# Kernel tuning notes

Hardware: AMD Instinct MI355X
Metric: run time of the kernel (lower is better)

The kernel has to match this reference:

```python
import jax, jax.numpy as jnp
import numpy as np

B, S, H, NH, DH, F, L = 4, 2048, 512, 8, 64, 2048, 4
ALPHA = 1.0   # config.lag_time_scale_alpha
EPS = 1e-12   # BERT layer_norm_eps
MS_PER_MIN = 60.0 * 1000.0


def setup_inputs() -> dict:
    key = jax.random.key(0)
    ks = jax.random.split(key, 24)
    p = lambda k, shape: (jax.random.normal(k, shape, jnp.float32) * 0.02)
    inp = {
        "query_states": jax.random.normal(ks[0], (B, S, H), jnp.float32),
        "attention_mask": jnp.zeros((B, 1, 1, S), jnp.float32),
        "position_bias": jax.random.normal(ks[1], (1, NH, S, S), jnp.float32) * 0.02,
        "timestamp": jnp.sort(jax.random.randint(ks[2], (B, S), 0, 36_000_000, jnp.int32), axis=-1),
        # stacked per-layer parameters (L leading dim)
        "wq": p(ks[3], (L, H, H)), "bq": jnp.zeros((L, H), jnp.float32),
        "wk": p(ks[4], (L, H, H)), "bk": jnp.zeros((L, H), jnp.float32),
        "wv": p(ks[5], (L, H, H)), "bv": jnp.zeros((L, H), jnp.float32),
        "wo": p(ks[6], (L, H, H)), "bo": jnp.zeros((L, H), jnp.float32),
        "ln1_g": jnp.ones((L, H), jnp.float32), "ln1_b": jnp.zeros((L, H), jnp.float32),
        "wi": p(ks[7], (L, H, F)), "bi": jnp.zeros((L, F), jnp.float32),
        "wo2": p(ks[8], (L, F, H)), "bo2": jnp.zeros((L, H), jnp.float32),
        "ln2_g": jnp.ones((L, H), jnp.float32), "ln2_b": jnp.zeros((L, H), jnp.float32),
    }
    return inp


def _ln(x, g, b):
    m = x.mean(-1, keepdims=True)
    v = ((x - m) ** 2).mean(-1, keepdims=True)
    return (x - m) / jnp.sqrt(v + EPS) * g + b


def reference(query_states, attention_mask, position_bias, timestamp,
              wq, bq, wk, bk, wv, bv, wo, bo, ln1_g, ln1_b,
              wi, bi, wo2, bo2, ln2_g, ln2_b):
    # encoder (is_decoder=False) lag-time scale: (B,1,S,S)
    lag = (timestamp[:, None, :, None] - timestamp[:, None, None, :]).astype(jnp.float32) / MS_PER_MIN
    scale = np.sqrt(DH).astype(np.float32) - ALPHA / (jnp.clip(lag, 0.0) + 1.0) + ALPHA

    x = query_states
    for l in range(L):
        def proj(w, b):
            return (x @ w + b).reshape(B, S, NH, DH).transpose(0, 2, 1, 3)  # (B,NH,S,DH)
        q, k, v = proj(wq[l], bq[l]), proj(wk[l], bk[l]), proj(wv[l], bv[l])
        scores = jnp.einsum('bhqd,bhkd->bhqk', q, k) / scale + position_bias + attention_mask
        probs = jax.nn.softmax(scores, axis=-1)
        ctx = jnp.einsum('bhqk,bhkd->bhqd', probs, v).transpose(0, 2, 1, 3).reshape(B, S, H)
        attn = _ln(ctx @ wo[l] + bo[l] + x, ln1_g[l], ln1_b[l])
        ffn = jax.nn.gelu(attn @ wi[l] + bi[l], approximate=False) @ wo2[l] + bo2[l]
        x = _ln(ffn + attn, ln2_g[l], ln2_b[l])
    return x
```

## Files before the change

kernel.cpp:

```cpp
#include <hip/hip_runtime.h>
#include <stdint.h>

typedef unsigned short u16;
using short8  = __attribute__((ext_vector_type(8))) short;
using float4v = __attribute__((ext_vector_type(4))) float;

#define L2E 1.4426950408889634f

__device__ inline float4v f4zero() { float4v z = {0.f, 0.f, 0.f, 0.f}; return z; }

__device__ inline u16 f2bf(float f) {
  union { float f; uint32_t i; } v; v.f = f;
  uint32_t r = v.i + 0x7fffu + ((v.i >> 16) & 1u);
  return (u16)(r >> 16);
}
__device__ inline float bf2f(u16 h) {
  union { uint32_t i; float f; } v; v.i = ((uint32_t)h) << 16; return v.f;
}

__device__ inline void glds16(const u16* g, u16* lds_base, int lane) {
#if __has_builtin(__builtin_amdgcn_global_load_lds)
  (void)lane;
  __builtin_amdgcn_global_load_lds((const __attribute__((address_space(1))) void*)g,
                                   (__attribute__((address_space(3))) void*)lds_base,
                                   16, 0, 0);
#else
  *(uint4*)(lds_base + (size_t)lane * 8) = *(const uint4*)g;
#endif
}

__global__ __launch_bounds__(256) void transpose_cast_kernel(
    const float* __restrict__ in, u16* __restrict__ out, int K, int N, size_t out_ls) {
  __shared__ float tile[32][33];
  const int tx = threadIdx.x & 31, ty = threadIdx.x >> 5;
  in  += (size_t)blockIdx.z * K * N;
  out += (size_t)blockIdx.z * out_ls;
  const int n  = blockIdx.x * 32 + tx;
  const int k0 = blockIdx.y * 32;
#pragma unroll
  for (int j = 0; j < 32; j += 8)
    tile[ty + j][tx] = in[(size_t)(k0 + ty + j) * N + n];
  __syncthreads();
  const int k = k0 + tx;
  const int n0 = blockIdx.x * 32;
#pragma unroll
  for (int j = 0; j < 32; j += 8)
    out[(size_t)(n0 + ty + j) * K + k] = f2bf(tile[tx][ty + j]);
}

__global__ __launch_bounds__(256) void cast_kernel(const float* __restrict__ in,
                                                   u16* __restrict__ out) {
  const int i = (blockIdx.x * 256 + threadIdx.x) * 4;
  float4 t = *(const float4*)(in + i);
  ushort4 o;
  o.x = f2bf(t.x); o.y = f2bf(t.y); o.z = f2bf(t.z); o.w = f2bf(t.w);
  *(ushort4*)(out + i) = o;
}

__global__ __launch_bounds__(256) void pb_tile_kernel(const float* __restrict__ pb,
                                                      u16* __restrict__ pbT) {
  const int g  = blockIdx.x * 256 + threadIdx.x;
  const int mm = g & 15;
  const int q  = (g >> 4) & 2047;
  const int kbh = g >> 15;
  const int kb = kbh & 31, h = kbh >> 5;
  const float* src = pb + ((size_t)h * 2048 + q) * 2048 + kb * 64 + mm;
  ushort4 o;
  o.x = f2bf(src[0]  * L2E);
  o.y = f2bf(src[16] * L2E);
  o.z = f2bf(src[32] * L2E);
  o.w = f2bf(src[48] * L2E);
  *(ushort4*)(pbT + ((size_t)(h * 32 + kb) * 2048 + q) * 64 + mm * 4) = o;
}

__global__ __launch_bounds__(256) void maskts_kernel(const float* __restrict__ mask,
                                                     const int* __restrict__ ts,
                                                     float* __restrict__ maskE,
                                                     float* __restrict__ tsf) {
  const int i = blockIdx.x * 256 + threadIdx.x;
  maskE[i] = mask[i] * L2E;
  tsf[i]   = (float)ts[i];
}

template <int BM, int BN, int NN, int KK, int EPI>
__global__ __launch_bounds__(256) void gemm_kernel(
    const u16* __restrict__ A, const u16* __restrict__ Wt,
    const float* __restrict__ b0, const float* __restrict__ b1, const float* __restrict__ b2,
    const u16* __restrict__ resid,
    void* __restrict__ o0, void* __restrict__ o1, void* __restrict__ o2) {
  constexpr int FI = BM / 32;
  constexpr int FJB = BN / 32;
  constexpr int FIW = BM / 32;
  constexpr int FJW = BN / 32;
  __shared__ __align__(16) u16 As[BM * 64];
  __shared__ __align__(16) u16 Bs[BN * 64];
  const int tid = threadIdx.x, lane = tid & 63, wv = tid >> 6;
  const int quad = lane >> 4, mm = lane & 15;
  const int m0 = blockIdx.x * BM, n0 = blockIdx.y * BN;
  const int wm = (wv >> 1) * (BM / 2), wn = (wv & 1) * (BN / 2);
  const int srow = tid >> 3, slot = tid & 7;
  const int chunk = slot ^ (srow & 7);
  const u16* Ag = A  + (size_t)(m0 + srow) * KK + chunk * 8;
  const u16* Bg = Wt + (size_t)(n0 + srow) * KK + chunk * 8;
  u16* AsW = As + (size_t)(wv * 8) * 64;
  u16* BsW = Bs + (size_t)(wv * 8) * 64;
  const int sw = mm & 7;

  float4v acc[FIW][FJW];
#pragma unroll
  for (int i = 0; i < FIW; i++)
#pragma unroll
    for (int j = 0; j < FJW; j++) acc[i][j] = f4zero();

  for (int kt = 0; kt < KK; kt += 64) {
#pragma unroll
    for (int i = 0; i < FI; i++)
      glds16(Ag + (size_t)i * 32 * KK + kt, AsW + i * 32 * 64, lane);
#pragma unroll
    for (int j = 0; j < FJB; j++)
      glds16(Bg + (size_t)j * 32 * KK + kt, BsW + j * 32 * 64, lane);
    __syncthreads();
#pragma unroll
    for (int ks = 0; ks < 2; ks++) {
      short8 a[FIW], b[FJW];
#pragma unroll
      for (int i = 0; i < FIW; i++)
        a[i] = *(const short8*)(As + (size_t)(wm + i * 16 + mm) * 64 + (size_t)((ks * 4 + quad) ^ sw) * 8);
#pragma unroll
      for (int j = 0; j < FJW; j++)
        b[j] = *(const short8*)(Bs + (size_t)(wn + j * 16 + mm) * 64 + (size_t)((ks * 4 + quad) ^ sw) * 8);
#pragma unroll
      for (int i = 0; i < FIW; i++)
#pragma unroll
        for (int j = 0; j < FJW; j++)
          acc[i][j] = __builtin_amdgcn_mfma_f32_16x16x32_bf16(a[i], b[j], acc[i][j], 0, 0, 0);
    }
    __syncthreads();
  }

#pragma unroll
  for (int j = 0; j < FJW; j++) {
    const int gn = n0 + wn + j * 16 + mm;
    if (EPI == 4) {
      const int which = gn >> 9, col = gn & 511, h = (gn >> 6) & 7, d = gn & 63;
      const float* bp = (which == 0) ? b0 : (which == 1) ? b1 : b2;
      const float bias = bp[col];
      u16* dst = (which == 0) ? (u16*)o0 : (which == 1) ? (u16*)o1 : (u16*)o2;
#pragma unroll
      for (int i = 0; i < FIW; i++)
#pragma unroll
        for (int r = 0; r < 4; r++) {
          const int gm = m0 + wm + i * 16 + quad * 4 + r;
          const int b_ = gm >> 11, s_ = gm & 2047;
          const float val = acc[i][j][r] + bias;
          if (which < 2)
            dst[((size_t)((b_ * 8 + h) * 2048 + s_)) * 64 + d] = f2bf(val);
          else
            dst[((size_t)((b_ * 8 + h) * 64 + d)) * 2048 + s_] = f2bf(val);
        }
    } else {
      const float bias = b0[gn];
#pragma unroll
      for (int i = 0; i < FIW; i++)
#pragma unroll
        for (int r = 0; r < 4; r++) {
          const int gm = m0 + wm + i * 16 + quad * 4 + r;
          const float val = acc[i][j][r] + bias;
          const size_t idx = (size_t)gm * NN + gn;
          if (EPI == 2) {
            ((float*)o0)[idx] = val + bf2f(resid[idx]);
          } else {
            const float z  = val * 0.70710678118654752f;
            const float az = fabsf(z);
            const float t  = __builtin_amdgcn_rcpf(1.0f + 0.3275911f * az);
            const float poly = t * (0.254829592f + t * (-0.284496736f +
                               t * (1.421413741f + t * (-1.453152027f + t * 1.061405429f))));
            const float e = __builtin_amdgcn_exp2f(-az * az * L2E);
            float erf_ = 1.0f - poly * e;
            erf_ = (z < 0.0f) ? -erf_ : erf_;
            ((u16*)o0)[idx] = f2bf(val * 0.5f * (1.0f + erf_));
          }
        }
    }
  }
}

template <bool TILED>
__global__ __launch_bounds__(256) void flash3_kernel(
    const u16* __restrict__ Q, const u16* __restrict__ Kb, const u16* __restrict__ Vt,
    const u16* __restrict__ pbT, const float* __restrict__ pb32,
    const float* __restrict__ maskE, const float* __restrict__ tsf,
    u16* __restrict__ ctx) {
  __shared__ __align__(16) u16 Kls[64 * 64];
  __shared__ __align__(16) u16 Vls[64 * 64];
  __shared__ __align__(16) u16 P[4][16 * 72];
  const int tid = threadIdx.x, lane = tid & 63, w = tid >> 6;
  const int quad = lane >> 4, mm = lane & 15;
  const int bh = blockIdx.y, b_ = bh >> 3, h_ = bh & 7;
  const int q0 = blockIdx.x * 64 + w * 16;
  const size_t qk_base = (size_t)bh * 2048 * 64;
  const size_t v_base  = (size_t)bh * 64 * 2048;
  const int srow = lane >> 3, slot = lane & 7;
  const int chunk = slot ^ srow;
  const int sw = mm & 7;

  short8 aq[2];
#pragma unroll
  for (int t = 0; t < 2; t++)
    aq[t] = *(const short8*)(Q + qk_base + (size_t)(q0 + mm) * 64 + t * 32 + quad * 8);

  float tqf[4];
#pragma unroll
  for (int r = 0; r < 4; r++) tqf[r] = tsf[b_ * 2048 + q0 + quad * 4 + r];

  float l_r[4] = {0.f, 0.f, 0.f, 0.f};
  float4v o[4];
#pragma unroll
  for (int ob = 0; ob < 4; ob++) o[ob] = f4zero();

  ushort4 pbc[4]; float tkc[4], mkc[4];
  if (TILED) {
#pragma unroll
    for (int r = 0; r < 4; r++)
      pbc[r] = *(const ushort4*)(pbT + ((size_t)(h_ * 32) * 2048 + q0 + quad * 4 + r) * 64 + mm * 4);
  }
#pragma unroll
  for (int nb = 0; nb < 4; nb++) {
    tkc[nb] = tsf[b_ * 2048 + nb * 16 + mm];
    mkc[nb] = maskE[b_ * 2048 + nb * 16 + mm];
  }

  for (int kt = 0; kt < 32; kt++) {
    const int k0 = kt * 64;
    __syncthreads();
#pragma unroll
    for (int i = 0; i < 2; i++) {
      const int row = w * 16 + i * 8 + srow;
      glds16(Kb + qk_base + (size_t)(k0 + row) * 64 + chunk * 8, Kls + (w * 16 + i * 8) * 64, lane);
      glds16(Vt + v_base + (size_t)row * 2048 + k0 + chunk * 8, Vls + (w * 16 + i * 8) * 64, lane);
    }
    __syncthreads();

    float4v s[4];
#pragma unroll
    for (int nb = 0; nb < 4; nb++) {
      const short8 kf0 = *(const short8*)(Kls + (size_t)(nb * 16 + mm) * 64 + (size_t)(quad ^ sw) * 8);
      const short8 kf1 = *(const short8*)(Kls + (size_t)(nb * 16 + mm) * 64 + (size_t)((4 + quad) ^ sw) * 8);
      s[nb] = __builtin_amdgcn_mfma_f32_16x16x32_bf16(aq[0], kf0, f4zero(), 0, 0, 0);
      s[nb] = __builtin_amdgcn_mfma_f32_16x16x32_bf16(aq[1], kf1, s[nb], 0, 0, 0);
    }

    const int kn = (kt < 31) ? kt + 1 : kt;
    ushort4 pbn[4]; float tkn[4], mkn[4];
    if (TILED) {
#pragma unroll
      for (int r = 0; r < 4; r++)
        pbn[r] = *(const ushort4*)(pbT + ((size_t)(h_ * 32 + kn) * 2048 + q0 + quad * 4 + r) * 64 + mm * 4);
    }
#pragma unroll
    for (int nb = 0; nb < 4; nb++) {
      tkn[nb] = tsf[b_ * 2048 + kn * 64 + nb * 16 + mm];
      mkn[nb] = maskE[b_ * 2048 + kn * 64 + nb * 16 + mm];
    }

#pragma unroll
    for (int r = 0; r < 4; r++) {
      float pbv[4];
      if (TILED) {
        pbv[0] = bf2f(pbc[r].x); pbv[1] = bf2f(pbc[r].y);
        pbv[2] = bf2f(pbc[r].z); pbv[3] = bf2f(pbc[r].w);
      } else {
#pragma unroll
        for (int nb = 0; nb < 4; nb++)
          pbv[nb] = pb32[((size_t)h_ * 2048 + q0 + quad * 4 + r) * 2048 + k0 + nb * 16 + mm] * L2E;
      }
#pragma unroll
      for (int nb = 0; nb < 4; nb++) {
        const float u = fmaxf(tqf[r] - tkc[nb], 0.f);
        const float invE = fmaf(u, L2E, 86561.70245333781f) *
                           __builtin_amdgcn_rcpf(fmaf(u, 9.f, 480000.f));
        const float t = fmaf(s[nb][r], invE, pbv[nb] + mkc[nb]);
        const float p = __builtin_amdgcn_exp2f(t);
        l_r[r] += p;
        P[w][(quad * 4 + r) * 72 + nb * 16 + mm] = f2bf(p);
      }
    }

    const short8 ap0 = *(const short8*)(&P[w][mm * 72 + quad * 8]);
    const short8 ap1 = *(const short8*)(&P[w][mm * 72 + 32 + quad * 8]);
#pragma unroll
    for (int ob = 0; ob < 4; ob++) {
      const short8 vf0 = *(const short8*)(Vls + (size_t)(ob * 16 + mm) * 64 + (size_t)(quad ^ sw) * 8);
      const short8 vf1 = *(const short8*)(Vls + (size_t)(ob * 16 + mm) * 64 + (size_t)((4 + quad) ^ sw) * 8);
      o[ob] = __builtin_amdgcn_mfma_f32_16x16x32_bf16(ap0, vf0, o[ob], 0, 0, 0);
      o[ob] = __builtin_amdgcn_mfma_f32_16x16x32_bf16(ap1, vf1, o[ob], 0, 0, 0);
    }
#pragma unroll
    for (int r = 0; r < 4; r++) pbc[r] = pbn[r];
#pragma unroll
    for (int nb = 0; nb < 4; nb++) { tkc[nb] = tkn[nb]; mkc[nb] = mkn[nb]; }
  }

#pragma unroll
  for (int r = 0; r < 4; r++) {
    float l = l_r[r];
#pragma unroll
    for (int sh = 1; sh < 16; sh <<= 1) l += __shfl_xor(l, sh, 64);
    const float rl = __builtin_amdgcn_rcpf(l);
    const int qrow = q0 + quad * 4 + r;
#pragma unroll
    for (int ob = 0; ob < 4; ob++)
      ctx[((size_t)b_ * 2048 + qrow) * 512 + h_ * 64 + ob * 16 + mm] = f2bf(o[ob][r] * rl);
  }
}

__global__ __launch_bounds__(256) void ln_kernel(
    const float* __restrict__ in, const float* __restrict__ g, const float* __restrict__ bb,
    float* __restrict__ of, u16* __restrict__ obf) {
  const int lane = threadIdx.x & 63, w = threadIdx.x >> 6;
  const int row = blockIdx.x * 4 + w;
  const float* x = in + (size_t)row * 512;
  float v[8];
  const float4 t0 = *(const float4*)(x + lane * 8);
  const float4 t1 = *(const float4*)(x + lane * 8 + 4);
  v[0] = t0.x; v[1] = t0.y; v[2] = t0.z; v[3] = t0.w;
  v[4] = t1.x; v[5] = t1.y; v[6] = t1.z; v[7] = t1.w;
  float s = 0.f;
#pragma unroll
  for (int i = 0; i < 8; i++) s += v[i];
#pragma unroll
  for (int sh = 1; sh < 64; sh <<= 1) s += __shfl_xor(s, sh, 64);
  const float mean = s * (1.0f / 512.0f);
  float sq = 0.f;
#pragma unroll
  for (int i = 0; i < 8; i++) { const float d = v[i] - mean; sq += d * d; }
#pragma unroll
  for (int sh = 1; sh < 64; sh <<= 1) sq += __shfl_xor(sq, sh, 64);
  const float rstd = rsqrtf(sq * (1.0f / 512.0f) + 1e-12f);
#pragma unroll
  for (int i = 0; i < 8; i++) {
    const int col = lane * 8 + i;
    const float y = (v[i] - mean) * rstd * g[col] + bb[col];
    if (of) of[(size_t)row * 512 + col] = y;
    obf[(size_t)row * 512 + col] = f2bf(y);
  }
}

extern "C" void kernel_launch(void* const* d_in, const int* in_sizes, int n_in,
                              void* d_out, int out_size, void* d_ws, size_t ws_size,
                              hipStream_t stream) {
  const float* x_in = (const float*)d_in[0];
  const float* mask = (const float*)d_in[1];
  const float* pb   = (const float*)d_in[2];
  const int*   ts   = (const int*)d_in[3];
  const float* wq = (const float*)d_in[4];  const float* bq = (const float*)d_in[5];
  const float* wk = (const float*)d_in[6];  const float* bk = (const float*)d_in[7];
  const float* wvp = (const float*)d_in[8]; const float* bv = (const float*)d_in[9];
  const float* wo = (const float*)d_in[10]; const float* bo = (const float*)d_in[11];
  const float* ln1g = (const float*)d_in[12]; const float* ln1b = (const float*)d_in[13];
  const float* wi = (const float*)d_in[14]; const float* bi = (const float*)d_in[15];
  const float* wo2 = (const float*)d_in[16]; const float* bo2 = (const float*)d_in[17];
  const float* ln2g = (const float*)d_in[18]; const float* ln2b = (const float*)d_in[19];

  char* ws = (char*)d_ws;
  const size_t o_wqkv  = 0;
  const size_t o_woT   = 6291456;
  const size_t o_wiT   = 8388608;
  const size_t o_wo2T  = 16777216;
  const size_t o_maskE = 25165824;
  const size_t o_tsf   = 25198592;
  const size_t o_xbf   = 25231360;
  const size_t o_qb    = 33619968;
  const size_t o_kb    = 42008576;
  const size_t o_vb    = 50397184;
  const size_t o_ctx   = 58785792;
  const size_t o_attnb = 67174400;
  const size_t o_tmp   = 75563008;
  const size_t o_pbT   = 92340224;
  const bool tiled = ws_size >= (o_pbT + 67108864ull);

  u16*   wqkvT = (u16*)(ws + o_wqkv);
  u16*   woT   = (u16*)(ws + o_woT);
  u16*   wiT   = (u16*)(ws + o_wiT);
  u16*   wo2T  = (u16*)(ws + o_wo2T);
  float* maskE = (float*)(ws + o_maskE);
  float* tsf   = (float*)(ws + o_tsf);
  u16*   xbf   = (u16*)(ws + o_xbf);
  u16*   qb    = (u16*)(ws + o_qb);
  u16*   kb    = (u16*)(ws + o_kb);
  u16*   vb    = (u16*)(ws + o_vb);
  u16*   ctx   = (u16*)(ws + o_ctx);
  u16*   hb    = (u16*)(ws + o_qb);
  u16*   attnb = (u16*)(ws + o_attnb);
  float* tmp   = (float*)(ws + o_tmp);
  u16*   pbT   = (u16*)(ws + o_pbT);

  const dim3 blk(256);
  transpose_cast_kernel<<<dim3(16, 16, 4), blk, 0, stream>>>(wq,  wqkvT,          512, 512, 786432);
  transpose_cast_kernel<<<dim3(16, 16, 4), blk, 0, stream>>>(wk,  wqkvT + 262144, 512, 512, 786432);
  transpose_cast_kernel<<<dim3(16, 16, 4), blk, 0, stream>>>(wvp, wqkvT + 524288, 512, 512, 786432);
  transpose_cast_kernel<<<dim3(16, 16, 4), blk, 0, stream>>>(wo,  woT,  512, 512,  262144);
  transpose_cast_kernel<<<dim3(64, 16, 4), blk, 0, stream>>>(wi,  wiT,  512, 2048, 1048576);
  transpose_cast_kernel<<<dim3(16, 64, 4), blk, 0, stream>>>(wo2, wo2T, 2048, 512, 1048576);
  maskts_kernel<<<32, blk, 0, stream>>>(mask, ts, maskE, tsf);
  cast_kernel<<<4096, blk, 0, stream>>>(x_in, xbf);
  if (tiled) pb_tile_kernel<<<32768, blk, 0, stream>>>(pb, pbT);

  for (int l = 0; l < 4; l++) {
    gemm_kernel<128, 128, 1536, 512, 4><<<dim3(64, 12), blk, 0, stream>>>(
        xbf, wqkvT + (size_t)l * 786432, bq + l * 512, bk + l * 512, bv + l * 512,
        nullptr, qb, kb, vb);
    if (tiled)
      flash3_kernel<true><<<dim3(32, 32), blk, 0, stream>>>(qb, kb, vb, pbT, pb, maskE, tsf, ctx);
    else
      flash3_kernel<false><<<dim3(32, 32), blk, 0, stream>>>(qb, kb, vb, nullptr, pb, maskE, tsf, ctx);
    gemm_kernel<128, 64, 512, 512, 2><<<dim3(64, 8), blk, 0, stream>>>(
        ctx, woT + (size_t)l * 262144, bo + l * 512, nullptr, nullptr, xbf,
        tmp, nullptr, nullptr);
    ln_kernel<<<2048, blk, 0, stream>>>(tmp, ln1g + l * 512, ln1b + l * 512, nullptr, attnb);
    gemm_kernel<128, 128, 2048, 512, 3><<<dim3(64, 16), blk, 0, stream>>>(
        attnb, wiT + (size_t)l * 1048576, bi + l * 2048, nullptr, nullptr, nullptr,
        hb, nullptr, nullptr);
    gemm_kernel<128, 64, 512, 2048, 2><<<dim3(64, 8), blk, 0, stream>>>(
        hb, wo2T + (size_t)l * 1048576, bo2 + l * 512, nullptr, nullptr, attnb,
        tmp, nullptr, nullptr);
    ln_kernel<<<2048, blk, 0, stream>>>(tmp, ln2g + l * 512, ln2b + l * 512,
                                        (l == 3) ? (float*)d_out : nullptr, xbf);
  }
  (void)in_sizes; (void)n_in; (void)out_size;
}
```

Measured before the change: 1.373 ms.

## Switch bf16 to fp16 and precompute tiled lag-scale inverse table

All bf16 storage and MFMA calls become fp16, which gives more mantissa bits at the same throughput. A new inv_tile_kernel precomputes the per-(batch,q,k) inverse lag scale once into an fp16 tiled buffer. The flash kernel then loads it alongside the position bias and no longer computes rcp per element in each of the four layers. This adds 32MB of workspace and extra memory traffic per attention pass, and fp16 brings an overflow risk for large activations.

```diff
diff --git a/kernel.cpp b/kernel.cpp
--- a/kernel.cpp
+++ b/kernel.cpp
@@ -2,20 +2,18 @@
 #include <stdint.h>
 
 typedef unsigned short u16;
-using short8  = __attribute__((ext_vector_type(8))) short;
+using half8   = __attribute__((ext_vector_type(8))) _Float16;
 using float4v = __attribute__((ext_vector_type(4))) float;
 
 #define L2E 1.4426950408889634f
 
 __device__ inline float4v f4zero() { float4v z = {0.f, 0.f, 0.f, 0.f}; return z; }
 
-__device__ inline u16 f2bf(float f) {
-  union { float f; uint32_t i; } v; v.f = f;
-  uint32_t r = v.i + 0x7fffu + ((v.i >> 16) & 1u);
-  return (u16)(r >> 16);
-}
-__device__ inline float bf2f(u16 h) {
-  union { uint32_t i; float f; } v; v.i = ((uint32_t)h) << 16; return v.f;
+__device__ inline u16 f2h(float f) {
+  union { _Float16 h; u16 u; } v; v.h = (_Float16)f; return v.u;
+}
+__device__ inline float h2f(u16 u) {
+  union { u16 u; _Float16 h; } v; v.u = u; return (float)v.h;
 }
 
 __device__ inline void glds16(const u16* g, u16* lds_base, int lane) {
@@ -45,7 +43,7 @@
   const int n0 = blockIdx.x * 32;
 #pragma unroll
   for (int j = 0; j < 32; j += 8)
-    out[(size_t)(n0 + ty + j) * K + k] = f2bf(tile[tx][ty + j]);
+    out[(size_t)(n0 + ty + j) * K + k] = f2h(tile[tx][ty + j]);
 }
 
 __global__ __launch_bounds__(256) void cast_kernel(const float* __restrict__ in,
@@ -53,7 +51,7 @@
   const int i = (blockIdx.x * 256 + threadIdx.x) * 4;
   float4 t = *(const float4*)(in + i);
   ushort4 o;
-  o.x = f2bf(t.x); o.y = f2bf(t.y); o.z = f2bf(t.z); o.w = f2bf(t.w);
+  o.x = f2h(t.x); o.y = f2h(t.y); o.z = f2h(t.z); o.w = f2h(t.w);
   *(ushort4*)(out + i) = o;
 }
 
@@ -66,11 +64,32 @@
   const int kb = kbh & 31, h = kbh >> 5;
   const float* src = pb + ((size_t)h * 2048 + q) * 2048 + kb * 64 + mm;
   ushort4 o;
-  o.x = f2bf(src[0]  * L2E);
-  o.y = f2bf(src[16] * L2E);
-  o.z = f2bf(src[32] * L2E);
-  o.w = f2bf(src[48] * L2E);
+  o.x = f2h(src[0]  * L2E);
+  o.y = f2h(src[16] * L2E);
+  o.z = f2h(src[32] * L2E);
+  o.w = f2h(src[48] * L2E);
   *(ushort4*)(pbT + ((size_t)(h * 32 + kb) * 2048 + q) * 64 + mm * 4) = o;
+}
+
+__global__ __launch_bounds__(256) void inv_tile_kernel(const int* __restrict__ ts,
+                                                       u16* __restrict__ invT) {
+  const int g  = blockIdx.x * 256 + threadIdx.x;
+  const int mm = g & 15;
+  const int q  = (g >> 4) & 2047;
+  const int kb = (g >> 15) & 31;
+  const int b  = g >> 20;
+  const int tq = ts[b * 2048 + q];
+  ushort4 o;
+  u16* op = (u16*)&o;
+#pragma unroll
+  for (int nb = 0; nb < 4; nb++) {
+    const int k = kb * 64 + nb * 16 + mm;
+    const int du = tq - ts[b * 2048 + k];
+    const float u = (du > 0) ? (float)du : 0.f;
+    op[nb] = f2h(fmaf(u, L2E, 86561.70245333781f) *
+                 __builtin_amdgcn_rcpf(fmaf(u, 9.f, 480000.f)));
+  }
+  *(ushort4*)(invT + ((size_t)(b * 32 + kb) * 2048 + q) * 64 + mm * 4) = o;
 }
 
 __global__ __launch_bounds__(256) void maskts_kernel(const float* __restrict__ mask,
@@ -122,18 +141,18 @@
     __syncthreads();
 #pragma unroll
     for (int ks = 0; ks < 2; ks++) {
-      short8 a[FIW], b[FJW];
+      half8 a[FIW], b[FJW];
 #pragma unroll
       for (int i = 0; i < FIW; i++)
-        a[i] = *(const short8*)(As + (size_t)(wm + i * 16 + mm) * 64 + (size_t)((ks * 4 + quad) ^ sw) * 8);
+        a[i] = *(const half8*)(As + (size_t)(wm + i * 16 + mm) * 64 + (size_t)((ks * 4 + quad) ^ sw) * 8);
 #pragma unroll
       for (int j = 0; j < FJW; j++)
-        b[j] = *(const short8*)(Bs + (size_t)(wn + j * 16 + mm) * 64 + (size_t)((ks * 4 + quad) ^ sw) * 8);
+        b[j] = *(const half8*)(Bs + (size_t)(wn + j * 16 + mm) * 64 + (size_t)((ks * 4 + quad) ^ sw) * 8);
 #pragma unroll
       for (int i = 0; i < FIW; i++)
 #pragma unroll
         for (int j = 0; j < FJW; j++)
-          acc[i][j] = __builtin_amdgcn_mfma_f32_16x16x32_bf16(a[i], b[j], acc[i][j], 0, 0, 0);
+          acc[i][j] = __builtin_amdgcn_mfma_f32_16x16x32_f16(a[i], b[j], acc[i][j], 0, 0, 0);
     }
     __syncthreads();
   }
@@ -154,9 +173,9 @@
           const int b_ = gm >> 11, s_ = gm & 2047;
           const float val = acc[i][j][r] + bias;
           if (which < 2)
-            dst[((size_t)((b_ * 8 + h) * 2048 + s_)) * 64 + d] = f2bf(val);
+            dst[((size_t)((b_ * 8 + h) * 2048 + s_)) * 64 + d] = f2h(val);
           else
-            dst[((size_t)((b_ * 8 + h) * 64 + d)) * 2048 + s_] = f2bf(val);
+            dst[((size_t)((b_ * 8 + h) * 64 + d)) * 2048 + s_] = f2h(val);
         }
     } else {
       const float bias = b0[gn];
@@ -168,7 +187,7 @@
           const float val = acc[i][j][r] + bias;
           const size_t idx = (size_t)gm * NN + gn;
           if (EPI == 2) {
-            ((float*)o0)[idx] = val + bf2f(resid[idx]);
+            ((float*)o0)[idx] = val + h2f(resid[idx]);
           } else {
             const float z  = val * 0.70710678118654752f;
             const float az = fabsf(z);
@@ -178,17 +197,18 @@
             const float e = __builtin_amdgcn_exp2f(-az * az * L2E);
             float erf_ = 1.0f - poly * e;
             erf_ = (z < 0.0f) ? -erf_ : erf_;
-            ((u16*)o0)[idx] = f2bf(val * 0.5f * (1.0f + erf_));
+            ((u16*)o0)[idx] = f2h(val * 0.5f * (1.0f + erf_));
           }
         }
     }
   }
 }
 
-template <bool TILED>
-__global__ __launch_bounds__(256) void flash3_kernel(
+template <int TILED>
+__global__ __launch_bounds__(256) void flash4_kernel(
     const u16* __restrict__ Q, const u16* __restrict__ Kb, const u16* __restrict__ Vt,
-    const u16* __restrict__ pbT, const float* __restrict__ pb32,
+    const u16* __restrict__ pbT, const u16* __restrict__ invT,
+    const float* __restrict__ pb32,
     const float* __restrict__ maskE, const float* __restrict__ tsf,
     u16* __restrict__ ctx) {
   __shared__ __align__(16) u16 Kls[64 * 64];
@@ -204,31 +224,38 @@
   const int chunk = slot ^ srow;
   const int sw = mm & 7;
 
-  short8 aq[2];
+  half8 aq[2];
 #pragma unroll
   for (int t = 0; t < 2; t++)
-    aq[t] = *(const short8*)(Q + qk_base + (size_t)(q0 + mm) * 64 + t * 32 + quad * 8);
+    aq[t] = *(const half8*)(Q + qk_base + (size_t)(q0 + mm) * 64 + t * 32 + quad * 8);
 
   float tqf[4];
-#pragma unroll
-  for (int r = 0; r < 4; r++) tqf[r] = tsf[b_ * 2048 + q0 + quad * 4 + r];
+  if (TILED < 2) {
+#pragma unroll
+    for (int r = 0; r < 4; r++) tqf[r] = tsf[b_ * 2048 + q0 + quad * 4 + r];
+  }
 
   float l_r[4] = {0.f, 0.f, 0.f, 0.f};
   float4v o[4];
 #pragma unroll
   for (int ob = 0; ob < 4; ob++) o[ob] = f4zero();
 
-  ushort4 pbc[4]; float tkc[4], mkc[4];
-  if (TILED) {
+  ushort4 pbc[4], invc[4]; float tkc[4], mkc[4];
+  if (TILED >= 1) {
 #pragma unroll
     for (int r = 0; r < 4; r++)
       pbc[r] = *(const ushort4*)(pbT + ((size_t)(h_ * 32) * 2048 + q0 + quad * 4 + r) * 64 + mm * 4);
   }
-#pragma unroll
-  for (int nb = 0; nb < 4; nb++) {
-    tkc[nb] = tsf[b_ * 2048 + nb * 16 + mm];
-    mkc[nb] = maskE[b_ * 2048 + nb * 16 + mm];
-  }
+  if (TILED == 2) {
+#pragma unroll
+    for (int r = 0; r < 4; r++)
+      invc[r] = *(const ushort4*)(invT + ((size_t)(b_ * 32) * 2048 + q0 + quad * 4 + r) * 64 + mm * 4);
+  } else {
+#pragma unroll
+    for (int nb = 0; nb < 4; nb++) tkc[nb] = tsf[b_ * 2048 + nb * 16 + mm];
+  }
+#pragma unroll
+  for (int nb = 0; nb < 4; nb++) mkc[nb] = maskE[b_ * 2048 + nb * 16 + mm];
 
   for (int kt = 0; kt < 32; kt++) {
     const int k0 = kt * 64;
@@ -244,59 +271,72 @@
     float4v s[4];
 #pragma unroll
     for (int nb = 0; nb < 4; nb++) {
-      const short8 kf0 = *(const short8*)(Kls + (size_t)(nb * 16 + mm) * 64 + (size_t)(quad ^ sw) * 8);
-      const short8 kf1 = *(const short8*)(Kls + (size_t)(nb * 16 + mm) * 64 + (size_t)((4 + quad) ^ sw) * 8);
-      s[nb] = __builtin_amdgcn_mfma_f32_16x16x32_bf16(aq[0], kf0, f4zero(), 0, 0, 0);
-      s[nb] = __builtin_amdgcn_mfma_f32_16x16x32_bf16(aq[1], kf1, s[nb], 0, 0, 0);
+      const half8 kf0 = *(const half8*)(Kls + (size_t)(nb * 16 + mm) * 64 + (size_t)(quad ^ sw) * 8);
+      const half8 kf1 = *(const half8*)(Kls + (size_t)(nb * 16 + mm) * 64 + (size_t)((4 + quad) ^ sw) * 8);
+      s[nb] = __builtin_amdgcn_mfma_f32_16x16x32_f16(aq[0], kf0, f4zero(), 0, 0, 0);
+      s[nb] = __builtin_amdgcn_mfma_f32_16x16x32_f16(aq[1], kf1, s[nb], 0, 0, 0);
     }
 
     const int kn = (kt < 31) ? kt + 1 : kt;
-    ushort4 pbn[4]; float tkn[4], mkn[4];
-    if (TILED) {
+    ushort4 pbn[4], invn[4]; float tkn[4], mkn[4];
+    if (TILED >= 1) {
 #pragma unroll
       for (int r = 0; r < 4; r++)
         pbn[r] = *(const ushort4*)(pbT + ((size_t)(h_ * 32 + kn) * 2048 + q0 + quad * 4 + r) * 64 + mm * 4);
     }
-#pragma unroll
-    for (int nb = 0; nb < 4; nb++) {
-      tkn[nb] = tsf[b_ * 2048 + kn * 64 + nb * 16 + mm];
-      mkn[nb] = maskE[b_ * 2048 + kn * 64 + nb * 16 + mm];
-    }
+    if (TILED == 2) {
+#pragma unroll
+      for (int r = 0; r < 4; r++)
+        invn[r] = *(const ushort4*)(invT + ((size_t)(b_ * 32 + kn) * 2048 + q0 + quad * 4 + r) * 64 + mm * 4);
+    } else {
+#pragma unroll
+      for (int nb = 0; nb < 4; nb++) tkn[nb] = tsf[b_ * 2048 + kn * 64 + nb * 16 + mm];
+    }
+#pragma unroll
+    for (int nb = 0; nb < 4; nb++) mkn[nb] = maskE[b_ * 2048 + kn * 64 + nb * 16 + mm];
 
 #pragma unroll
     for (int r = 0; r < 4; r++) {
-      float pbv[4];
-      if (TILED) {
-        pbv[0] = bf2f(pbc[r].x); pbv[1] = bf2f(pbc[r].y);
-        pbv[2] = bf2f(pbc[r].z); pbv[3] = bf2f(pbc[r].w);
+      float pbv[4], iv[4];
+      if (TILED >= 1) {
+        pbv[0] = h2f(pbc[r].x); pbv[1] = h2f(pbc[r].y);
+        pbv[2] = h2f(pbc[r].z); pbv[3] = h2f(pbc[r].w);
       } else {
 #pragma unroll
         for (int nb = 0; nb < 4; nb++)
           pbv[nb] = pb32[((size_t)h_ * 2048 + q0 + quad * 4 + r) * 2048 + k0 + nb * 16 + mm] * L2E;
       }
+      if (TILED == 2) {
+        iv[0] = h2f(invc[r].x); iv[1] = h2f(invc[r].y);
+        iv[2] = h2f(invc[r].z); iv[3] = h2f(invc[r].w);
+      } else {
+#pragma unroll
+        for (int nb = 0; nb < 4; nb++) {
+          const float u = fmaxf(tqf[r] - tkc[nb], 0.f);
+          iv[nb] = fmaf(u, L2E, 86561.70245333781f) *
+                   __builtin_amdgcn_rcpf(fmaf(u, 9.f, 480000.f));
+        }
+      }
 #pragma unroll
       for (int nb = 0; nb < 4; nb++) {
-        const float u = fmaxf(tqf[r] - tkc[nb], 0.f);
-        const float invE = fmaf(u, L2E, 86561.70245333781f) *
-                           __builtin_amdgcn_rcpf(fmaf(u, 9.f, 480000.f));
-        const float t = fmaf(s[nb][r], invE, pbv[nb] + mkc[nb]);
+        const float t = fmaf(s[nb][r], iv[nb], pbv[nb] + mkc[nb]);
         const float p = __builtin_amdgcn_exp2f(t);
         l_r[r] += p;
-        P[w][(quad * 4 + r) * 72 + nb * 16 + mm] = f2bf(p);
+        P[w][(quad * 4 + r) * 72 + nb * 16 + mm] = f2h(p);
       }
     }
 
-    const short8 ap0 = *(const short8*)(&P[w][mm * 72 + quad * 8]);
-    const short8 ap1 = *(const short8*)(&P[w][mm * 72 + 32 + quad * 8]);
+    const half8 ap0 = *(const half8*)(&P[w][mm * 72 + quad * 8]);
+    const half8 ap1 = *(const half8*)(&P[w][mm * 72 + 32 + quad * 8]);
 #pragma unroll
     for (int ob = 0; ob < 4; ob++) {
-      const short8 vf0 = *(const short8*)(Vls + (size_t)(ob * 16 + mm) * 64 + (size_t)(quad ^ sw) * 8);
-      const short8 vf1 = *(const short8*)(Vls + (size_t)(ob * 16 + mm) * 64 + (size_t)((4 + quad) ^ sw) * 8);
-      o[ob] = __builtin_amdgcn_mfma_f32_16x16x32_bf16(ap0, vf0, o[ob], 0, 0, 0);
-      o[ob] = __builtin_amdgcn_mfma_f32_16x16x32_bf16(ap1, vf1, o[ob], 0, 0, 0);
-    }
-#pragma unroll
-    for (int r = 0; r < 4; r++) pbc[r] = pbn[r];
+      const half8 vf0 = *(const half8*)(Vls + (size_t)(ob * 16 + mm) * 64 + (size_t)(quad ^ sw) * 8);
+      const half8 vf1 = *(const half8*)(Vls + (size_t)(ob * 16 + mm) * 64 + (size_t)((4 + quad) ^ sw) * 8);
+      o[ob] = __builtin_amdgcn_mfma_f32_16x16x32_f16(ap0, vf0, o[ob], 0, 0, 0);
+      o[ob] = __builtin_amdgcn_mfma_f32_16x16x32_f16(ap1, vf1, o[ob], 0, 0, 0);
+    }
+#pragma unroll
+    for (int r = 0; r < 4; r++) { pbc[r] = pbn[r]; invc[r] = invn[r]; }
 #pragma unroll
     for (int nb = 0; nb < 4; nb++) { tkc[nb] = tkn[nb]; mkc[nb] = mkn[nb]; }
   }
@@ -310,7 +350,7 @@
     const int qrow = q0 + quad * 4 + r;
 #pragma unroll
     for (int ob = 0; ob < 4; ob++)
-      ctx[((size_t)b_ * 2048 + qrow) * 512 + h_ * 64 + ob * 16 + mm] = f2bf(o[ob][r] * rl);
+      ctx[((size_t)b_ * 2048 + qrow) * 512 + h_ * 64 + ob * 16 + mm] = f2h(o[ob][r] * rl);
   }
 }
 
@@ -342,7 +382,7 @@
     const int col = lane * 8 + i;
     const float y = (v[i] - mean) * rstd * g[col] + bb[col];
     if (of) of[(size_t)row * 512 + col] = y;
-    obf[(size_t)row * 512 + col] = f2bf(y);
+    obf[(size_t)row * 512 + col] = f2h(y);
   }
 }
 
@@ -377,7 +417,9 @@
   const size_t o_attnb = 67174400;
   const size_t o_tmp   = 75563008;
   const size_t o_pbT   = 92340224;
-  const bool tiled = ws_size >= (o_pbT + 67108864ull);
+  const size_t o_invT  = 159449088;
+  const int tiled = (ws_size >= o_invT + 33554432ull) ? 2
+                  : (ws_size >= o_pbT + 67108864ull) ? 1 : 0;
 
   u16*   wqkvT = (u16*)(ws + o_wqkv);
   u16*   woT   = (u16*)(ws + o_woT);
@@ -394,6 +436,7 @@
   u16*   attnb = (u16*)(ws + o_attnb);
   float* tmp   = (float*)(ws + o_tmp);
   u16*   pbT   = (u16*)(ws + o_pbT);
+  u16*   invT  = (u16*)(ws + o_invT);
 
   const dim3 blk(256);
   transpose_cast_kernel<<<dim3(16, 16, 4), blk, 0, stream>>>(wq,  wqkvT,          512, 512, 786432);
@@ -404,16 +447,19 @@
   transpose_cast_kernel<<<dim3(16, 64, 4), blk, 0, stream>>>(wo2, wo2T, 2048, 512, 1048576);
   maskts_kernel<<<32, blk, 0, stream>>>(mask, ts, maskE, tsf);
   cast_kernel<<<4096, blk, 0, stream>>>(x_in, xbf);
-  if (tiled) pb_tile_kernel<<<32768, blk, 0, stream>>>(pb, pbT);
+  if (tiled >= 1) pb_tile_kernel<<<32768, blk, 0, stream>>>(pb, pbT);
+  if (tiled == 2) inv_tile_kernel<<<16384, blk, 0, stream>>>(ts, invT);
 
   for (int l = 0; l < 4; l++) {
     gemm_kernel<128, 128, 1536, 512, 4><<<dim3(64, 12), blk, 0, stream>>>(
         xbf, wqkvT + (size_t)l * 786432, bq + l * 512, bk + l * 512, bv + l * 512,
         nullptr, qb, kb, vb);
-    if (tiled)
-      flash3_kernel<true><<<dim3(32, 32), blk, 0, stream>>>(qb, kb, vb, pbT, pb, maskE, tsf, ctx);
+    if (tiled == 2)
+      flash4_kernel<2><<<dim3(32, 32), blk, 0, stream>>>(qb, kb, vb, pbT, invT, pb, maskE, tsf, ctx);
+    else if (tiled == 1)
+      flash4_kernel<1><<<dim3(32, 32), blk, 0, stream>>>(qb, kb, vb, pbT, nullptr, pb, maskE, tsf, ctx);
     else
-      flash3_kernel<false><<<dim3(32, 32), blk, 0, stream>>>(qb, kb, vb, nullptr, pb, maskE, tsf, ctx);
+      flash4_kernel<0><<<dim3(32, 32), blk, 0, stream>>>(qb, kb, vb, nullptr, nullptr, pb, maskE, tsf, ctx);
     gemm_kernel<128, 64, 512, 512, 2><<<dim3(64, 8), blk, 0, stream>>>(
         ctx, woT + (size_t)l * 262144, bo + l * 512, nullptr, nullptr, xbf,
         tmp, nullptr, nullptr);
```

Result: no change. 1.368 ms (-0.3%).
